# Kernel optimization log

Measured on AMD Instinct MI355X. Metric: run time of the kernel, lower is better.

## Reference

```python
import jax, jax.numpy as jnp
import numpy as np

EPS_NORM = 1e-8
EPS_Q = 1e-5

def rmsnorm(x, g):
    var = jnp.mean(x * x, axis=-1, keepdims=True)
    return x * jax.lax.rsqrt(var + EPS_NORM) * g

def activation_quant(x):
    # per-token int8 absmax quantization
    scale = 127.0 / jnp.clip(jnp.max(jnp.abs(x), axis=-1, keepdims=True), EPS_Q, None)
    return jnp.clip(jnp.round(x * scale), -128.0, 127.0) / scale

def weight_quant(w):
    # per-tensor ternary absmean quantization
    scale = 1.0 / jnp.clip(jnp.mean(jnp.abs(w)), EPS_Q, None)
    return jnp.clip(jnp.round(w * scale), -1.0, 1.0) / scale

def ste(x, qfn):
    # straight-through estimator: forward quantized, backward identity
    return x + jax.lax.stop_gradient(qfn(x) - x)

def bitlinear(x, w, g):
    h = rmsnorm(x, g)
    hq = ste(h, activation_quant)
    wq = ste(w, weight_quant)
    return jnp.einsum('bsh,oh->bso', hq, wq)

def setup_inputs() -> dict:
    key = jax.random.key(0)
    k1, k2, k3 = jax.random.split(key, 3)
    B, S, H = 2, 2048, 2048
    I = int(H * 4.0)  # intermediate_size = 8192
    x = jax.random.normal(k1, (B, S, H), dtype=jnp.float32)
    w_gate = jax.random.normal(k2, (2 * I, H), dtype=jnp.float32) * 0.02
    g_gate = jnp.ones((H,), dtype=jnp.float32)
    w_down = jax.random.normal(k3, (H, I), dtype=jnp.float32) * 0.02
    g_down = jnp.ones((I,), dtype=jnp.float32)
    return {"x": x, "w_gate": w_gate, "g_gate": g_gate, "w_down": w_down, "g_down": g_down}

def reference(x, w_gate, g_gate, w_down, g_down):
    y = bitlinear(x, w_gate, g_gate)        # [B,S,2I]
    gate, up = jnp.split(y, 2, axis=-1)     # each [B,S,I]
    z = bitlinear(jax.nn.silu(gate) * up, w_down, g_down)  # [B,S,H]
    return z
```

## Files before the change

kernel.cpp:

```cpp
#include <hip/hip_runtime.h>
#include <hip/hip_bf16.h>
#include <hip/hip_fp16.h>

#define DEVINL __device__ __forceinline__

typedef float f32x4 __attribute__((ext_vector_type(4)));
typedef int i32x4 __attribute__((ext_vector_type(4)));
typedef unsigned int u32x4 __attribute__((ext_vector_type(4)));
typedef unsigned int u32x2 __attribute__((ext_vector_type(2)));

typedef __attribute__((address_space(1))) void void_g;
typedef __attribute__((address_space(3))) void void_l;

DEVINL void gload16(const void* g, void* l) {
  __builtin_amdgcn_global_load_lds((void_g*)g, (void_l*)l, 16, 0, 0);
}

DEVINL float wave_sum(float v) {
  #pragma unroll
  for (int o = 32; o > 0; o >>= 1) v += __shfl_down(v, o, 64);
  return v;
}
DEVINL float wave_max(float v) {
  #pragma unroll
  for (int o = 32; o > 0; o >>= 1) v = fmaxf(v, __shfl_down(v, o, 64));
  return v;
}

DEVINL unsigned int pack4(float a, float b, float c, float d) {
  return ((unsigned int)(unsigned char)(signed char)(int)a)
       | (((unsigned int)(unsigned char)(signed char)(int)b) << 8)
       | (((unsigned int)(unsigned char)(signed char)(int)c) << 16)
       | (((unsigned int)(unsigned char)(signed char)(int)d) << 24);
}

__global__ __launch_bounds__(256) void absum_kernel(const float* __restrict__ w,
                                                    long long nchunk, double* __restrict__ out) {
  long long stride = (long long)gridDim.x * 256;
  long long i = (long long)blockIdx.x * 256 + threadIdx.x;
  float s = 0.f;
  for (; i < nchunk; i += stride) {
    f32x4 v = ((const f32x4*)w)[i];
    s += fabsf(v[0]) + fabsf(v[1]) + fabsf(v[2]) + fabsf(v[3]);
  }
  s = wave_sum(s);
  __shared__ float red[4];
  int lane = threadIdx.x & 63, wv = threadIdx.x >> 6;
  if (lane == 0) red[wv] = s;
  __syncthreads();
  if (threadIdx.x == 0) atomicAdd(out, (double)(red[0] + red[1] + red[2] + red[3]));
}

__global__ __launch_bounds__(256) void quantw_kernel(const float* __restrict__ w,
                                                     signed char* __restrict__ tern,
                                                     long long nchunk,
                                                     const double* __restrict__ sum, double inv_n) {
  float scale = (float)(1.0 / fmax(*sum * inv_n, 1e-5));
  long long stride = (long long)gridDim.x * 256;
  long long i = (long long)blockIdx.x * 256 + threadIdx.x;
  for (; i < nchunk; i += stride) {
    f32x4 v0 = ((const f32x4*)w)[2 * i];
    f32x4 v1 = ((const f32x4*)w)[2 * i + 1];
    float t[8];
    #pragma unroll
    for (int k = 0; k < 4; k++) {
      t[k]     = fminf(fmaxf(rintf(v0[k] * scale), -1.f), 1.f);
      t[4 + k] = fminf(fmaxf(rintf(v1[k] * scale), -1.f), 1.f);
    }
    u32x2 o;
    o[0] = pack4(t[0], t[1], t[2], t[3]);
    o[1] = pack4(t[4], t[5], t[6], t[7]);
    ((u32x2*)tern)[i] = o;
  }
}

__global__ __launch_bounds__(256) void actq1_kernel(const float* __restrict__ x,
                                                    const float* __restrict__ g,
                                                    signed char* __restrict__ q,
                                                    float* __restrict__ a) {
  int t = blockIdx.x, tid = threadIdx.x;
  int lane = tid & 63, wv = tid >> 6;
  __shared__ float redS[4], redM[4];

  const f32x4* xr = (const f32x4*)(x + (size_t)t * 2048);
  f32x4 v0 = xr[tid * 2], v1 = xr[tid * 2 + 1];
  float ssq = 0.f;
  #pragma unroll
  for (int k = 0; k < 4; k++) ssq += v0[k] * v0[k] + v1[k] * v1[k];
  float ws_ = wave_sum(ssq);
  if (lane == 0) redS[wv] = ws_;
  __syncthreads();
  float tot = redS[0] + redS[1] + redS[2] + redS[3];
  float r = rsqrtf(tot / 2048.f + 1e-8f);

  f32x4 g0 = ((const f32x4*)g)[tid * 2], g1 = ((const f32x4*)g)[tid * 2 + 1];
  float h[8], amax = 0.f;
  #pragma unroll
  for (int k = 0; k < 4; k++) {
    h[k]     = v0[k] * r * g0[k];
    h[4 + k] = v1[k] * r * g1[k];
    amax = fmaxf(amax, fmaxf(fabsf(h[k]), fabsf(h[4 + k])));
  }
  float wm = wave_max(amax);
  if (lane == 0) redM[wv] = wm;
  __syncthreads();
  float am = fmaxf(fmaxf(fmaxf(redM[0], redM[1]), fmaxf(redM[2], redM[3])), 1e-5f);
  float scale = 127.f / am;

  float qv[8];
  #pragma unroll
  for (int k = 0; k < 8; k++) qv[k] = fminf(fmaxf(rintf(h[k] * scale), -128.f), 127.f);
  u32x2 o;
  o[0] = pack4(qv[0], qv[1], qv[2], qv[3]);
  o[1] = pack4(qv[4], qv[5], qv[6], qv[7]);
  ((u32x2*)(q + (size_t)t * 2048))[tid] = o;
  if (tid == 0) a[t] = am / 127.f;
}

__global__ __launch_bounds__(256) void silu_rms_q_kernel(const unsigned short* __restrict__ y,
                                                         const float* __restrict__ g,
                                                         signed char* __restrict__ q2,
                                                         float* __restrict__ a2) {
  int t = blockIdx.x, tid = threadIdx.x;
  int lane = tid & 63, wv = tid >> 6;
  __shared__ float redS[4], redM[4];
  const u32x4* gate = (const u32x4*)(y + (size_t)t * 16384);
  const u32x4* up   = (const u32x4*)(y + (size_t)t * 16384 + 8192);

  float v[32];
  float ssq = 0.f;
  #pragma unroll
  for (int b = 0; b < 4; b++) {
    u32x4 gr = gate[b * 256 + tid];
    u32x4 ur = up[b * 256 + tid];
    #pragma unroll
    for (int k = 0; k < 4; k++) {
      float g0 = __half2float(__ushort_as_half((unsigned short)(gr[k] & 0xFFFFu)));
      float g1 = __half2float(__ushort_as_half((unsigned short)(gr[k] >> 16)));
      float u0 = __half2float(__ushort_as_half((unsigned short)(ur[k] & 0xFFFFu)));
      float u1 = __half2float(__ushort_as_half((unsigned short)(ur[k] >> 16)));
      float v0 = g0 / (1.f + expf(-g0)) * u0;
      float v1 = g1 / (1.f + expf(-g1)) * u1;
      v[b * 8 + 2 * k] = v0;
      v[b * 8 + 2 * k + 1] = v1;
      ssq += v0 * v0 + v1 * v1;
    }
  }
  float ws_ = wave_sum(ssq);
  if (lane == 0) redS[wv] = ws_;
  __syncthreads();
  float tot = redS[0] + redS[1] + redS[2] + redS[3];
  float r = rsqrtf(tot / 8192.f + 1e-8f);

  float amax = 0.f;
  #pragma unroll
  for (int b = 0; b < 4; b++) {
    f32x4 ga = ((const f32x4*)g)[b * 512 + tid * 2];
    f32x4 gb = ((const f32x4*)g)[b * 512 + tid * 2 + 1];
    #pragma unroll
    for (int k = 0; k < 4; k++) {
      float h0 = v[b * 8 + k]     * r * ga[k];
      float h1 = v[b * 8 + 4 + k] * r * gb[k];
      v[b * 8 + k] = h0;
      v[b * 8 + 4 + k] = h1;
      amax = fmaxf(amax, fmaxf(fabsf(h0), fabsf(h1)));
    }
  }
  float wm = wave_max(amax);
  if (lane == 0) redM[wv] = wm;
  __syncthreads();
  float am = fmaxf(fmaxf(fmaxf(redM[0], redM[1]), fmaxf(redM[2], redM[3])), 1e-5f);
  float scale = 127.f / am;

  #pragma unroll
  for (int b = 0; b < 4; b++) {
    float qv[8];
    #pragma unroll
    for (int k = 0; k < 8; k++)
      qv[k] = fminf(fmaxf(rintf(v[b * 8 + k] * scale), -128.f), 127.f);
    u32x2 o;
    o[0] = pack4(qv[0], qv[1], qv[2], qv[3]);
    o[1] = pack4(qv[4], qv[5], qv[6], qv[7]);
    ((u32x2*)(q2 + (size_t)t * 8192))[b * 256 + tid] = o;
  }
  if (tid == 0) a2[t] = am / 127.f;
}


#define RD16(P, off) (*(const i32x4*)((P) + (off)))
#define MFMA_I8(a, b, c) __builtin_amdgcn_mfma_i32_16x16x64_i8((a), (b), (c), 0, 0, 0)
#define VM0 asm volatile("s_waitcnt vmcnt(0)" ::: "memory");

#define CB(ks) ((((ks) << 6) | sq) ^ sfx)
#define RDA(d0_, d1_, d2_, d3_, h, ks) { const int o_ = arow0 + (h) * 8192 + CB(ks); \
  d0_ = RD16(Ac, o_); d1_ = RD16(Ac, o_ + 2048); d2_ = RD16(Ac, o_ + 4096); d3_ = RD16(Ac, o_ + 6144); }
#define RDB(d0_, d1_, d2_, d3_, ks) { const int o_ = brow0 + CB(ks); \
  d0_ = RD16(Bc, o_); d1_ = RD16(Bc, o_ + 2048); d2_ = RD16(Bc, o_ + 4096); d3_ = RD16(Bc, o_ + 6144); }

#define CL(h, A0_, A1_, A2_, A3_, B0_, B1_, B2_, B3_) \
  __builtin_amdgcn_s_setprio(1); \
  acc[(h)*4+0][0] = MFMA_I8(A0_, B0_, acc[(h)*4+0][0]); \
  acc[(h)*4+0][1] = MFMA_I8(A0_, B1_, acc[(h)*4+0][1]); \
  acc[(h)*4+0][2] = MFMA_I8(A0_, B2_, acc[(h)*4+0][2]); \
  acc[(h)*4+0][3] = MFMA_I8(A0_, B3_, acc[(h)*4+0][3]); \
  acc[(h)*4+1][0] = MFMA_I8(A1_, B0_, acc[(h)*4+1][0]); \
  acc[(h)*4+1][1] = MFMA_I8(A1_, B1_, acc[(h)*4+1][1]); \
  acc[(h)*4+1][2] = MFMA_I8(A1_, B2_, acc[(h)*4+1][2]); \
  acc[(h)*4+1][3] = MFMA_I8(A1_, B3_, acc[(h)*4+1][3]); \
  acc[(h)*4+2][0] = MFMA_I8(A2_, B0_, acc[(h)*4+2][0]); \
  acc[(h)*4+2][1] = MFMA_I8(A2_, B1_, acc[(h)*4+2][1]); \
  acc[(h)*4+2][2] = MFMA_I8(A2_, B2_, acc[(h)*4+2][2]); \
  acc[(h)*4+2][3] = MFMA_I8(A2_, B3_, acc[(h)*4+2][3]); \
  acc[(h)*4+3][0] = MFMA_I8(A3_, B0_, acc[(h)*4+3][0]); \
  acc[(h)*4+3][1] = MFMA_I8(A3_, B1_, acc[(h)*4+3][1]); \
  acc[(h)*4+3][2] = MFMA_I8(A3_, B2_, acc[(h)*4+3][2]); \
  acc[(h)*4+3][3] = MFMA_I8(A3_, B3_, acc[(h)*4+3][3]); \
  __builtin_amdgcn_s_setprio(0);

#define TILE_BODY(S1, S2, S3) { \
  i32x4 a0, a1, a2, a3, b0, b1, b2, b3, c0, c1, c2, c3, d0, d1, d2, d3; \
  RDA(a0, a1, a2, a3, 0, 0)             \
  RDB(b0, b1, b2, b3, 0)                \
  S1 \
  RDA(c0, c1, c2, c3, 1, 0)             \
  CL(0, a0, a1, a2, a3, b0, b1, b2, b3)               \
  RDA(d0, d1, d2, d3, 0, 1)             \
  RDB(a0, a1, a2, a3, 1)                \
  S2 \
  CL(1, c0, c1, c2, c3, b0, b1, b2, b3)               \
  RDA(b0, b1, b2, b3, 1, 1)             \
  S3 \
  CL(0, d0, d1, d2, d3, a0, a1, a2, a3)               \
  CL(1, b0, b1, b2, b3, a0, a1, a2, a3)               \
}

template <int OUT_MODE>
__global__ __launch_bounds__(512, 2) void gemm256_i8_kernel(
    const signed char* __restrict__ A, const signed char* __restrict__ B,
    void* __restrict__ Cv, int M, int N, int K,
    const float* __restrict__ rowscale, const double* __restrict__ wsum, double inv_n) {
  __shared__ __align__(16) signed char lds[131072];
  const int tid = threadIdx.x;
  const int lane = tid & 63;
  const int wid = tid >> 6;
  const int wr = wid >> 2;
  const int wc = wid & 3;

  const int nbn = N >> 8;
  const int b = blockIdx.x;
  const int cpx = gridDim.x >> 3;
  const int sb = (b & 7) * cpx + (b >> 3);
  const int m0 = (sb / nbn) << 8;
  const int n0 = (sb % nbn) << 8;

  const int fr = lane & 15;
  const int sq = (lane >> 4) << 4;
  const int sfx = (fr & 7) << 4;
  const int arow0 = (wr * 128 + fr) * 128;
  const int brow0 = (wc * 64 + fr) * 128;

  const int rr = tid >> 3;
  const int co = (((tid & 7) ^ (rr & 7)) << 4);
  const signed char* gA = A + (size_t)(m0 + rr) * K + co;
  const signed char* gB = B + (size_t)(n0 + rr) * K + co;
  const size_t g64 = (size_t)64 * K;

  i32x4 acc[8][4] = {};
  const int NT = K >> 7;

  {
    signed char* Ad = lds + tid * 16;
    signed char* Bd = Ad + 32768;
    gload16(gB,           Bd);
    gload16(gB + g64,     Bd + 8192);
    gload16(gB + 2 * g64, Bd + 16384);
    gload16(gB + 3 * g64, Bd + 24576);
    gload16(gA,           Ad);
    gload16(gA + g64,     Ad + 8192);
    gload16(gA + 2 * g64, Ad + 16384);
    gload16(gA + 3 * g64, Ad + 24576);
    VM0
    __builtin_amdgcn_s_barrier();
  }

  for (int t = 0; t < NT - 1; ++t) {
    const signed char* Ac = lds + ((t & 1) << 16);
    const signed char* Bc = Ac + 32768;
    signed char* Ad = lds + (((t & 1) ^ 1) << 16) + tid * 16;
    signed char* Bd = Ad + 32768;
    const signed char* gAt = gA + (size_t)(t + 1) * 128;
    const signed char* gBt = gB + (size_t)(t + 1) * 128;

    TILE_BODY(
      gload16(gBt, Bd); gload16(gBt + g64, Bd + 8192); gload16(gBt + 2 * g64, Bd + 16384); ,
      gload16(gBt + 3 * g64, Bd + 24576); gload16(gAt, Ad); gload16(gAt + 2 * g64, Ad + 16384); ,
      gload16(gAt + g64, Ad + 8192); gload16(gAt + 3 * g64, Ad + 24576); )

    VM0
    __builtin_amdgcn_s_barrier();
  }

  {
    const signed char* Ac = lds + (((NT - 1) & 1) << 16);
    const signed char* Bc = Ac + 32768;
    TILE_BODY(, , )
  }

  float sw = (float)fmax(*wsum * inv_n, 1e-5);
  const int qo = lane >> 4;
  const int cb = n0 + wc * 64 + fr;
  #pragma unroll
  for (int ai = 0; ai < 8; ai++) {
    const int rowb = m0 + wr * 128 + ai * 16 + qo * 4;
    #pragma unroll
    for (int r = 0; r < 4; r++) {
      float sc = rowscale[rowb + r] * sw;
      size_t off = (size_t)(rowb + r) * N + cb;
      #pragma unroll
      for (int n = 0; n < 4; n++) {
        float vv = (float)acc[ai][n][r] * sc;
        if (OUT_MODE == 0) ((unsigned short*)Cv)[off + n * 16] = __half_as_ushort(__float2half(vv));
        else               ((float*)Cv)[off + n * 16] = vv;
      }
    }
  }
}

extern "C" void kernel_launch(void* const* d_in, const int* in_sizes, int n_in,
                              void* d_out, int out_size, void* d_ws, size_t ws_size,
                              hipStream_t stream) {
  const float* x      = (const float*)d_in[0];
  const float* w_gate = (const float*)d_in[1];
  const float* g_gate = (const float*)d_in[2];
  const float* w_down = (const float*)d_in[3];
  const float* g_down = (const float*)d_in[4];
  float* out = (float*)d_out;

  char* ws = (char*)d_ws;
  double* sums = (double*)ws;
  float* a1 = (float*)(ws + 4096);
  float* a2 = (float*)(ws + 20480);
  const size_t MB = 1024 * 1024;
  signed char* tern_g = (signed char*)(ws + 65536);
  signed char* q2     = tern_g;
  signed char* tern_d = (signed char*)(ws + 65536 + 32 * MB);
  signed char* q1     = (signed char*)(ws + 65536 + 48 * MB);
  unsigned short* yh  = (unsigned short*)(ws + 65536 + 56 * MB);

  hipMemsetAsync(sums, 0, 16, stream);
  absum_kernel<<<2048, 256, 0, stream>>>(w_gate, 33554432LL / 4, sums + 0);
  absum_kernel<<<1024, 256, 0, stream>>>(w_down, 16777216LL / 4, sums + 1);
  quantw_kernel<<<4096, 256, 0, stream>>>(w_gate, tern_g, 33554432LL / 8, sums + 0, 1.0 / 33554432.0);
  quantw_kernel<<<2048, 256, 0, stream>>>(w_down, tern_d, 16777216LL / 8, sums + 1, 1.0 / 16777216.0);
  actq1_kernel<<<4096, 256, 0, stream>>>(x, g_gate, q1, a1);
  gemm256_i8_kernel<0><<<1024, 512, 0, stream>>>(q1, tern_g, yh, 4096, 16384, 2048,
                                                 a1, sums + 0, 1.0 / 33554432.0);
  silu_rms_q_kernel<<<4096, 256, 0, stream>>>(yh, g_down, q2, a2);
  gemm256_i8_kernel<1><<<128, 512, 0, stream>>>(q2, tern_d, out, 4096, 2048, 8192,
                                                a2, sums + 1, 1.0 / 16777216.0);
}
```

Before: 595.0 us.

## Add 128x256 int8 GEMM for down projection and stagger K-halves across waves

Adds a gemm128_i8_kernel with 128-row tiles, so the down-projection GEMM launches 256 blocks instead of 128 and fills more of the CUs. Both GEMM kernels now issue all global-to-LDS loads at the start of each tile. Odd and even waves read the two K halves in opposite order, which spreads LDS bank traffic. The smaller tile lowers arithmetic intensity per block and uses launch_bounds(512,1), which trades occupancy for more parallel blocks.

```diff
diff --git a/kernel.cpp b/kernel.cpp
--- a/kernel.cpp
+++ b/kernel.cpp
@@ -217,21 +217,19 @@
   acc[(h)*4+3][3] = MFMA_I8(A3_, B3_, acc[(h)*4+3][3]); \
   __builtin_amdgcn_s_setprio(0);
 
-#define TILE_BODY(S1, S2, S3) { \
+#define TILE_BODY(S, KA, KB) { \
   i32x4 a0, a1, a2, a3, b0, b1, b2, b3, c0, c1, c2, c3, d0, d1, d2, d3; \
-  RDA(a0, a1, a2, a3, 0, 0)             \
-  RDB(b0, b1, b2, b3, 0)                \
-  S1 \
-  RDA(c0, c1, c2, c3, 1, 0)             \
-  CL(0, a0, a1, a2, a3, b0, b1, b2, b3)               \
-  RDA(d0, d1, d2, d3, 0, 1)             \
-  RDB(a0, a1, a2, a3, 1)                \
-  S2 \
-  CL(1, c0, c1, c2, c3, b0, b1, b2, b3)               \
-  RDA(b0, b1, b2, b3, 1, 1)             \
-  S3 \
-  CL(0, d0, d1, d2, d3, a0, a1, a2, a3)               \
-  CL(1, b0, b1, b2, b3, a0, a1, a2, a3)               \
+  S \
+  RDA(a0, a1, a2, a3, 0, KA)              \
+  RDB(b0, b1, b2, b3, KA)                 \
+  RDA(c0, c1, c2, c3, 1, KA)              \
+  CL(0, a0, a1, a2, a3, b0, b1, b2, b3) \
+  RDA(d0, d1, d2, d3, 0, KB)              \
+  RDB(a0, a1, a2, a3, KB)                 \
+  CL(1, c0, c1, c2, c3, b0, b1, b2, b3) \
+  RDA(b0, b1, b2, b3, 1, KB)              \
+  CL(0, d0, d1, d2, d3, a0, a1, a2, a3) \
+  CL(1, b0, b1, b2, b3, a0, a1, a2, a3) \
 }
 
 template <int OUT_MODE>
@@ -283,6 +281,12 @@
     __builtin_amdgcn_s_barrier();
   }
 
+#define STAGE_ALL \
+    gload16(gBt, Bd); gload16(gBt + g64, Bd + 8192); \
+    gload16(gBt + 2 * g64, Bd + 16384); gload16(gBt + 3 * g64, Bd + 24576); \
+    gload16(gAt, Ad); gload16(gAt + g64, Ad + 8192); \
+    gload16(gAt + 2 * g64, Ad + 16384); gload16(gAt + 3 * g64, Ad + 24576);
+
   for (int t = 0; t < NT - 1; ++t) {
     const signed char* Ac = lds + ((t & 1) << 16);
     const signed char* Bc = Ac + 32768;
@@ -291,10 +295,8 @@
     const signed char* gAt = gA + (size_t)(t + 1) * 128;
     const signed char* gBt = gB + (size_t)(t + 1) * 128;
 
-    TILE_BODY(
-      gload16(gBt, Bd); gload16(gBt + g64, Bd + 8192); gload16(gBt + 2 * g64, Bd + 16384); ,
-      gload16(gBt + 3 * g64, Bd + 24576); gload16(gAt, Ad); gload16(gAt + 2 * g64, Ad + 16384); ,
-      gload16(gAt + g64, Ad + 8192); gload16(gAt + 3 * g64, Ad + 24576); )
+    if (wid & 1) { TILE_BODY(STAGE_ALL, 1, 0) }
+    else         { TILE_BODY(STAGE_ALL, 0, 1) }
 
     VM0
     __builtin_amdgcn_s_barrier();
@@ -303,7 +305,8 @@
   {
     const signed char* Ac = lds + (((NT - 1) & 1) << 16);
     const signed char* Bc = Ac + 32768;
-    TILE_BODY(, , )
+    if (wid & 1) { TILE_BODY(, 1, 0) }
+    else         { TILE_BODY(, 0, 1) }
   }
 
   float sw = (float)fmax(*wsum * inv_n, 1e-5);
@@ -326,6 +329,133 @@
   }
 }
 
+#define CL16(AA0, AA1, AA2, AA3, B0_, B1_, B2_, B3_) \
+  __builtin_amdgcn_s_setprio(1); \
+  acc[0][0] = MFMA_I8(AA0, B0_, acc[0][0]); \
+  acc[0][1] = MFMA_I8(AA0, B1_, acc[0][1]); \
+  acc[0][2] = MFMA_I8(AA0, B2_, acc[0][2]); \
+  acc[0][3] = MFMA_I8(AA0, B3_, acc[0][3]); \
+  acc[1][0] = MFMA_I8(AA1, B0_, acc[1][0]); \
+  acc[1][1] = MFMA_I8(AA1, B1_, acc[1][1]); \
+  acc[1][2] = MFMA_I8(AA1, B2_, acc[1][2]); \
+  acc[1][3] = MFMA_I8(AA1, B3_, acc[1][3]); \
+  acc[2][0] = MFMA_I8(AA2, B0_, acc[2][0]); \
+  acc[2][1] = MFMA_I8(AA2, B1_, acc[2][1]); \
+  acc[2][2] = MFMA_I8(AA2, B2_, acc[2][2]); \
+  acc[2][3] = MFMA_I8(AA2, B3_, acc[2][3]); \
+  acc[3][0] = MFMA_I8(AA3, B0_, acc[3][0]); \
+  acc[3][1] = MFMA_I8(AA3, B1_, acc[3][1]); \
+  acc[3][2] = MFMA_I8(AA3, B2_, acc[3][2]); \
+  acc[3][3] = MFMA_I8(AA3, B3_, acc[3][3]); \
+  __builtin_amdgcn_s_setprio(0);
+
+#define RDA2(d0_, d1_, d2_, d3_, ks) { const int o_ = arow0 + CB(ks); \
+  d0_ = RD16(Ac, o_); d1_ = RD16(Ac, o_ + 2048); d2_ = RD16(Ac, o_ + 4096); d3_ = RD16(Ac, o_ + 6144); }
+
+#define TILE_BODY2(S, KA, KB) { \
+  i32x4 a0, a1, a2, a3, b0, b1, b2, b3, c0, c1, c2, c3, d0, d1, d2, d3; \
+  S \
+  RDA2(a0, a1, a2, a3, KA)  RDB(b0, b1, b2, b3, KA) \
+  RDA2(c0, c1, c2, c3, KB) \
+  CL16(a0, a1, a2, a3, b0, b1, b2, b3) \
+  RDB(d0, d1, d2, d3, KB) \
+  CL16(c0, c1, c2, c3, d0, d1, d2, d3) \
+}
+
+template <int OUT_MODE>
+__global__ __launch_bounds__(512, 1) void gemm128_i8_kernel(
+    const signed char* __restrict__ A, const signed char* __restrict__ B,
+    void* __restrict__ Cv, int M, int N, int K,
+    const float* __restrict__ rowscale, const double* __restrict__ wsum, double inv_n) {
+  __shared__ __align__(16) signed char lds[98304];
+  const int tid = threadIdx.x;
+  const int lane = tid & 63;
+  const int wid = tid >> 6;
+  const int wr = wid >> 2;
+  const int wc = wid & 3;
+
+  const int nbn = N >> 8;
+  const int b = blockIdx.x;
+  const int cpx = gridDim.x >> 3;
+  const int sb = (b & 7) * cpx + (b >> 3);
+  const int m0 = (sb / nbn) << 7;
+  const int n0 = (sb % nbn) << 8;
+
+  const int fr = lane & 15;
+  const int sq = (lane >> 4) << 4;
+  const int sfx = (fr & 7) << 4;
+  const int arow0 = (wr * 64 + fr) * 128;
+  const int brow0 = (wc * 64 + fr) * 128;
+
+  const int rr = tid >> 3;
+  const int co = (((tid & 7) ^ (rr & 7)) << 4);
+  const signed char* gA = A + (size_t)(m0 + rr) * K + co;
+  const signed char* gB = B + (size_t)(n0 + rr) * K + co;
+  const size_t g64 = (size_t)64 * K;
+
+  i32x4 acc[4][4] = {};
+  const int NT = K >> 7;
+
+  {
+    signed char* Ad = lds + tid * 16;
+    signed char* Bd = Ad + 16384;
+    gload16(gB,           Bd);
+    gload16(gB + g64,     Bd + 8192);
+    gload16(gB + 2 * g64, Bd + 16384);
+    gload16(gB + 3 * g64, Bd + 24576);
+    gload16(gA,           Ad);
+    gload16(gA + g64,     Ad + 8192);
+    VM0
+    __builtin_amdgcn_s_barrier();
+  }
+
+#define STAGE_ALL2 \
+    gload16(gBt, Bd); gload16(gBt + g64, Bd + 8192); \
+    gload16(gBt + 2 * g64, Bd + 16384); gload16(gBt + 3 * g64, Bd + 24576); \
+    gload16(gAt, Ad); gload16(gAt + g64, Ad + 8192);
+
+  for (int t = 0; t < NT - 1; ++t) {
+    const signed char* Ac = lds + (t & 1) * 49152;
+    const signed char* Bc = Ac + 16384;
+    signed char* Ad = lds + ((t & 1) ^ 1) * 49152 + tid * 16;
+    signed char* Bd = Ad + 16384;
+    const signed char* gAt = gA + (size_t)(t + 1) * 128;
+    const signed char* gBt = gB + (size_t)(t + 1) * 128;
+
+    if (wid & 1) { TILE_BODY2(STAGE_ALL2, 1, 0) }
+    else         { TILE_BODY2(STAGE_ALL2, 0, 1) }
+
+    VM0
+    __builtin_amdgcn_s_barrier();
+  }
+
+  {
+    const signed char* Ac = lds + ((NT - 1) & 1) * 49152;
+    const signed char* Bc = Ac + 16384;
+    if (wid & 1) { TILE_BODY2(, 1, 0) }
+    else         { TILE_BODY2(, 0, 1) }
+  }
+
+  float sw = (float)fmax(*wsum * inv_n, 1e-5);
+  const int qo = lane >> 4;
+  const int cb = n0 + wc * 64 + fr;
+  #pragma unroll
+  for (int ai = 0; ai < 4; ai++) {
+    const int rowb = m0 + wr * 64 + ai * 16 + qo * 4;
+    #pragma unroll
+    for (int r = 0; r < 4; r++) {
+      float sc = rowscale[rowb + r] * sw;
+      size_t off = (size_t)(rowb + r) * N + cb;
+      #pragma unroll
+      for (int n = 0; n < 4; n++) {
+        float vv = (float)acc[ai][n][r] * sc;
+        if (OUT_MODE == 0) ((unsigned short*)Cv)[off + n * 16] = __half_as_ushort(__float2half(vv));
+        else               ((float*)Cv)[off + n * 16] = vv;
+      }
+    }
+  }
+}
+
 extern "C" void kernel_launch(void* const* d_in, const int* in_sizes, int n_in,
                               void* d_out, int out_size, void* d_ws, size_t ws_size,
                               hipStream_t stream) {
@@ -356,6 +486,6 @@
   gemm256_i8_kernel<0><<<1024, 512, 0, stream>>>(q1, tern_g, yh, 4096, 16384, 2048,
                                                  a1, sums + 0, 1.0 / 33554432.0);
   silu_rms_q_kernel<<<4096, 256, 0, stream>>>(yh, g_down, q2, a2);
-  gemm256_i8_kernel<1><<<128, 512, 0, stream>>>(q2, tern_d, out, 4096, 2048, 8192,
+  gemm128_i8_kernel<1><<<256, 512, 0, stream>>>(q2, tern_d, out, 4096, 2048, 8192,
                                                 a2, sums + 1, 1.0 / 16777216.0);
 }
```

New measurement: 591.8 us. About the same (-0.5%).
